# Kernel tuning notes

Hardware: AMD Instinct MI355X
Metric: run time of the kernel (lower is better)

The kernel has to match this reference:

```python
import jax, jax.numpy as jnp
import numpy as np

N_NODES = 50000
N_EDGES = 400000
N_GRAPHS = 128
IN_DIM = 768
HID = 128
N_CLASSES = 11
BN_EPS = 1e-5


def _sage_conv(x, src, dst, Wl, bl, Wr):
    # PyG SAGEConv (aggr='mean'): out = lin_l(mean_{j->i} x_j) + lin_r(x_i)
    # messages flow src -> dst; nodes with no in-edges get a zero aggregate.
    n = x.shape[0]
    deg = jax.ops.segment_sum(jnp.ones_like(dst, x.dtype), dst, num_segments=n)
    agg = jax.ops.segment_sum(x[src], dst, num_segments=n)  # [N, d] gather+scatter
    agg = agg / jnp.maximum(deg, 1.0)[:, None]
    return agg @ Wl.T + bl + x @ Wr.T


def _batch_norm(x, gamma, beta):
    # training-mode BatchNorm1d: biased batch statistics over the node axis
    m = jnp.mean(x, axis=0)
    v = jnp.var(x, axis=0)
    return (x - m) * jax.lax.rsqrt(v + BN_EPS) * gamma + beta


def setup_inputs() -> dict:
    key = jax.random.key(0)
    ks = jax.random.split(key, 16)
    x = jax.random.normal(ks[0], (N_NODES, IN_DIM), dtype=jnp.float32)
    edge_index = jax.random.randint(ks[1], (2, N_EDGES), 0, N_NODES, dtype=jnp.int32)
    batch = jnp.sort(jax.random.randint(ks[2], (N_NODES,), 0, N_GRAPHS, dtype=jnp.int32))

    def lin_w(k, out_d, in_d):
        return jax.random.normal(k, (out_d, in_d), dtype=jnp.float32) * (1.0 / np.sqrt(in_d))

    params = {
        'W1l': lin_w(ks[3], HID, IN_DIM), 'b1': jnp.zeros((HID,), jnp.float32),
        'W1r': lin_w(ks[4], HID, IN_DIM),
        'g1': jnp.ones((HID,), jnp.float32), 'be1': jnp.zeros((HID,), jnp.float32),
        'W2l': lin_w(ks[5], HID, HID), 'b2': jnp.zeros((HID,), jnp.float32),
        'W2r': lin_w(ks[6], HID, HID),
        'g2': jnp.ones((HID,), jnp.float32), 'be2': jnp.zeros((HID,), jnp.float32),
        'W3l': lin_w(ks[7], HID, HID), 'b3': jnp.zeros((HID,), jnp.float32),
        'W3r': lin_w(ks[8], HID, HID),
        'g3': jnp.ones((HID,), jnp.float32), 'be3': jnp.zeros((HID,), jnp.float32),
        'Wlin': lin_w(ks[9], N_CLASSES, HID), 'blin': jnp.zeros((N_CLASSES,), jnp.float32),
    }
    return {'x': x, 'edge_index': edge_index, 'batch': batch, **params}


def reference(x, edge_index, batch,
              W1l, b1, W1r, g1, be1,
              W2l, b2, W2r, g2, be2,
              W3l, b3, W3r, g3, be3,
              Wlin, blin):
    src, dst = edge_index[0], edge_index[1]
    h = jax.nn.relu(_batch_norm(_sage_conv(x, src, dst, W1l, b1, W1r), g1, be1))
    h = jax.nn.relu(_batch_norm(_sage_conv(h, src, dst, W2l, b2, W2r), g2, be2))
    h = _batch_norm(_sage_conv(h, src, dst, W3l, b3, W3r), g3, be3)
    # global_max_pool over graph ids
    pooled = jax.ops.segment_max(h, batch, num_segments=N_GRAPHS)  # [G, HID]
    # dropout is identity at inference
    return pooled @ Wlin.T + blin  # [G, 11]
```

## Files before the change

### kernel.cpp

```cpp
#include <hip/hip_runtime.h>

#define N_NODESC 50000
#define N_EDGESC 400000
#define N_GRAPHSC 128
#define IN_DIMC 768
#define HIDC 128
#define NCLSC 11
#define BN_EPSC 1e-5f
#define NB_AGG 8
#define NREP 64
#define SCAN_NB ((N_NODESC + 255) / 256)

typedef __bf16 bf16_t;
typedef __bf16 bf16x2 __attribute__((ext_vector_type(2)));
typedef __bf16 bf16x8 __attribute__((ext_vector_type(8)));
typedef float f32x4 __attribute__((ext_vector_type(4)));

typedef __attribute__((address_space(1))) void glb_void;
typedef __attribute__((address_space(3))) void lds_void;

__device__ __forceinline__ void cp16(const void* g, void* l) {
    __builtin_amdgcn_global_load_lds((glb_void*)g, (lds_void*)l, 16, 0, 0);
}

__device__ __forceinline__ f32x4 mfma_16x16x32_bf16(bf16x8 a, bf16x8 b, f32x4 c) {
    return __builtin_amdgcn_mfma_f32_16x16x32_bf16(a, b, c, 0, 0, 0);
}

template<int MODE, int KC>
__global__ __launch_bounds__(256) void gemm_kernel(const void* __restrict__ Av,
                                                   const bf16_t* __restrict__ Wb,
                                                   const float* __restrict__ sc,
                                                   bf16_t* __restrict__ Cl,
                                                   bf16_t* __restrict__ Cr,
                                                   int M)
{
    constexpr int NK   = KC / 32;
    constexpr int ASZ  = (MODE == 0) ? 16384 : 8192;
    constexpr int BSZ  = 8192;
    constexpr int NBB  = (MODE == 0) ? 2 : 3;
    constexpr int AISS = (MODE == 0) ? 4 : 2;
    constexpr int AKB  = (MODE == 0) ? 128 : 64;
    constexpr int SCSZ = (MODE == 1) ? 1024 : 0;
    __shared__ __align__(16) unsigned char smem[3 * ASZ + NBB * BSZ + SCSZ];
    unsigned char* Asm = smem;
    unsigned char* Bsm = smem + 3 * ASZ;
    float* scS = (float*)(smem + 3 * ASZ + NBB * BSZ);

    const int t    = threadIdx.x;
    const int m0   = blockIdx.x * 128;
    const int half = blockIdx.y;
    const int wid  = t >> 6;
    const int lane = t & 63;
    const int wm   = (wid >> 1) * 64;
    const int wn   = (wid & 1) * 64;
    const int l16  = lane & 15;
    const int quad = lane >> 4;

    const char* aSrc[AISS]; int aDst[AISS];
#pragma unroll
    for (int s = 0; s < AISS; s++) {
        int L = (s * 4 + wid) * 64 + lane;
        int r, c;
        if (MODE == 0) { r = L >> 3; c = (L & 7) ^ (r & 7); }
        else           { r = L >> 2; c = (L & 3) ^ ((r >> 1) & 3); }
        int row = m0 + r; if (row > M - 1) row = M - 1;
        if (MODE == 0) aSrc[s] = (const char*)Av + ((size_t)row * KC + (size_t)c * 4) * 4;
        else           aSrc[s] = (const char*)Av + ((size_t)row * KC + (size_t)c * 8) * 2;
        aDst[s] = (s * 4 + wid) * 1024;
    }
    const char* bSrc[2]; int bDst[2];
#pragma unroll
    for (int s = 0; s < 2; s++) {
        int L = (s * 4 + wid) * 64 + lane;
        int r = L >> 2;
        int c = (L & 3) ^ ((r >> 1) & 3);
        bSrc[s] = (const char*)(Wb + (size_t)(half * 128 + r) * KC + c * 8);
        bDst[s] = (s * 4 + wid) * 1024;
    }

    int aOff[4][2], bOff[4];
#pragma unroll
    for (int i = 0; i < 4; i++) {
        int ra = wm + i * 16 + l16;
        if (MODE == 0) {
            aOff[i][0] = ra * 128 + (((2 * quad)     ^ (ra & 7)) * 16);
            aOff[i][1] = ra * 128 + (((2 * quad + 1) ^ (ra & 7)) * 16);
        } else {
            aOff[i][0] = ra * 64 + ((quad ^ ((ra >> 1) & 3)) * 16);
            aOff[i][1] = 0;
        }
        int rb = wn + i * 16 + l16;
        bOff[i] = rb * 64 + ((quad ^ ((rb >> 1) & 3)) * 16);
    }

    if (MODE == 1) {
        scS[t] = sc[t];
        __syncthreads();
    }

#pragma unroll
    for (int s = 0; s < AISS; s++) cp16(aSrc[s], Asm + aDst[s]);
#pragma unroll
    for (int s = 0; s < 2; s++)    cp16(bSrc[s], Bsm + bDst[s]);
#pragma unroll
    for (int s = 0; s < AISS; s++) cp16(aSrc[s] + AKB, Asm + ASZ + aDst[s]);
    if (MODE == 1) {
#pragma unroll
        for (int s = 0; s < 2; s++) cp16(bSrc[s] + 64, Bsm + BSZ + bDst[s]);
    }

    f32x4 acc[4][4] = {};

    for (int it = 0; it < NK; ++it) {
        if (it + 2 < NK) {
            if constexpr (MODE == 0) {
                const size_t kb1 = (size_t)(it + 1) * 64;
                const int bb = (it + 1) & 1;
#pragma unroll
                for (int s = 0; s < 2; s++) cp16(bSrc[s] + kb1, Bsm + bb * BSZ + bDst[s]);
                const size_t ka2 = (size_t)(it + 2) * 128;
                const int ab = (it + 2) % 3;
#pragma unroll
                for (int s = 0; s < 4; s++) cp16(aSrc[s] + ka2, Asm + ab * ASZ + aDst[s]);
                asm volatile("s_waitcnt vmcnt(10)" ::: "memory");
            } else {
                const size_t kb2 = (size_t)(it + 2) * 64;
                const int nb = (it + 2) % 3;
#pragma unroll
                for (int s = 0; s < 2; s++) cp16(aSrc[s] + kb2, Asm + nb * ASZ + aDst[s]);
#pragma unroll
                for (int s = 0; s < 2; s++) cp16(bSrc[s] + kb2, Bsm + nb * BSZ + bDst[s]);
                asm volatile("s_waitcnt vmcnt(8)" ::: "memory");
            }
        } else if (it + 1 < NK) {
            if constexpr (MODE == 0) {
                const size_t kb1 = (size_t)(it + 1) * 64;
                const int bb = (it + 1) & 1;
#pragma unroll
                for (int s = 0; s < 2; s++) cp16(bSrc[s] + kb1, Bsm + bb * BSZ + bDst[s]);
                asm volatile("s_waitcnt vmcnt(6)" ::: "memory");
            } else {
                asm volatile("s_waitcnt vmcnt(4)" ::: "memory");
            }
        } else {
            asm volatile("s_waitcnt vmcnt(0)" ::: "memory");
        }
        asm volatile("s_barrier" ::: "memory");

        const unsigned char* Ab = Asm + (it % 3) * ASZ;
        const unsigned char* Bb = Bsm + ((MODE == 0) ? (it & 1) : (it % 3)) * BSZ;
        bf16x8 af[4], bfr[4];
        if constexpr (MODE == 0) {
#pragma unroll
            for (int i = 0; i < 4; i++) {
                float4 u0 = *(const float4*)(Ab + aOff[i][0]);
                float4 u1 = *(const float4*)(Ab + aOff[i][1]);
                af[i][0] = (bf16_t)u0.x; af[i][1] = (bf16_t)u0.y;
                af[i][2] = (bf16_t)u0.z; af[i][3] = (bf16_t)u0.w;
                af[i][4] = (bf16_t)u1.x; af[i][5] = (bf16_t)u1.y;
                af[i][6] = (bf16_t)u1.z; af[i][7] = (bf16_t)u1.w;
            }
        } else {
            float4 s0 = *(const float4*)&scS[it * 32 + quad * 8];
            float4 s1 = *(const float4*)&scS[it * 32 + quad * 8 + 4];
            float4 h0 = *(const float4*)&scS[HIDC + it * 32 + quad * 8];
            float4 h1 = *(const float4*)&scS[HIDC + it * 32 + quad * 8 + 4];
            float ss[8] = {s0.x, s0.y, s0.z, s0.w, s1.x, s1.y, s1.z, s1.w};
            float hh[8] = {h0.x, h0.y, h0.z, h0.w, h1.x, h1.y, h1.z, h1.w};
#pragma unroll
            for (int i = 0; i < 4; i++) {
                bf16x8 raw = *(const bf16x8*)(Ab + aOff[i][0]);
#pragma unroll
                for (int e = 0; e < 8; e++)
                    af[i][e] = (bf16_t)fmaxf(fmaf((float)raw[e], ss[e], hh[e]), 0.0f);
            }
        }
#pragma unroll
        for (int j = 0; j < 4; j++)
            bfr[j] = *(const bf16x8*)(Bb + bOff[j]);
#pragma unroll
        for (int i = 0; i < 4; i++)
#pragma unroll
            for (int j = 0; j < 4; j++)
                acc[i][j] = mfma_16x16x32_bf16(af[i], bfr[j], acc[i][j]);

        asm volatile("s_barrier" ::: "memory");
    }

    bf16_t* C = half ? Cr : Cl;
#pragma unroll
    for (int i = 0; i < 4; i++) {
        int rowb = m0 + wm + i * 16 + quad * 4;
#pragma unroll
        for (int j = 0; j < 4; j++) {
            int colh = wn + j * 16 + l16;
#pragma unroll
            for (int rr = 0; rr < 4; rr++) {
                int row = rowb + rr;
                if (row < M) C[(size_t)row * HIDC + colh] = (bf16_t)acc[i][j][rr];
            }
        }
    }
}

__global__ void init_kernel(const float* __restrict__ W1l, const float* __restrict__ W1r,
                            const float* __restrict__ W2l, const float* __restrict__ W2r,
                            const float* __restrict__ W3l, const float* __restrict__ W3r,
                            bf16_t* __restrict__ Wb1, bf16_t* __restrict__ Wb2,
                            bf16_t* __restrict__ Wb3,
                            int* __restrict__ degi, float* __restrict__ stats)
{
    const int NW1 = 128 * IN_DIMC;
    const int NW2 = 128 * HIDC;
    const int NS  = 3 * NREP * 256;
    int j = blockIdx.x * blockDim.x + threadIdx.x;
    if (j < 2 * NW1) { Wb1[j] = (bf16_t)((j < NW1) ? W1l[j] : W1r[j - NW1]); return; }
    j -= 2 * NW1;
    if (j < 2 * NW2) { Wb2[j] = (bf16_t)((j < NW2) ? W2l[j] : W2r[j - NW2]); return; }
    j -= 2 * NW2;
    if (j < 2 * NW2) { Wb3[j] = (bf16_t)((j < NW2) ? W3l[j] : W3r[j - NW2]); return; }
    j -= 2 * NW2;
    if (j < NS) { stats[j] = 0.0f; return; }
    j -= NS;
    if (j < N_NODESC) degi[j] = 0;
}

__global__ void degi_kernel(const int* __restrict__ ei, int* __restrict__ degi) {
    int e = blockIdx.x * blockDim.x + threadIdx.x;
    if (e < N_EDGESC) atomicAdd(&degi[ei[N_EDGESC + e]], 1);
}

__global__ __launch_bounds__(256) void scan1_kernel(const int* __restrict__ degi,
                                                    int* __restrict__ local,
                                                    int* __restrict__ partials)
{
    __shared__ int tmp[256];
    const int t = threadIdx.x;
    const int i = blockIdx.x * 256 + t;
    int v = (i < N_NODESC) ? degi[i] : 0;
    tmp[t] = v;
    __syncthreads();
    for (int off = 1; off < 256; off <<= 1) {
        int u = (t >= off) ? tmp[t - off] : 0;
        __syncthreads();
        tmp[t] += u;
        __syncthreads();
    }
    if (i < N_NODESC) local[i] = tmp[t] - v;
    if (t == 255) partials[blockIdx.x] = tmp[255];
}

__global__ __launch_bounds__(256) void scan2_kernel(int* __restrict__ partials)
{
    __shared__ int tmp[256];
    const int t = threadIdx.x;
    int v = (t < SCAN_NB) ? partials[t] : 0;
    tmp[t] = v;
    __syncthreads();
    for (int off = 1; off < 256; off <<= 1) {
        int u = (t >= off) ? tmp[t - off] : 0;
        __syncthreads();
        tmp[t] += u;
        __syncthreads();
    }
    if (t < SCAN_NB) partials[t] = tmp[t] - v;
}

__global__ __launch_bounds__(256) void scan3_kernel(const int* __restrict__ local,
                                                    const int* __restrict__ partials,
                                                    int* __restrict__ rowptr,
                                                    int* __restrict__ cursor)
{
    const int i = blockIdx.x * 256 + threadIdx.x;
    if (i < N_NODESC) {
        int r = local[i] + partials[blockIdx.x];
        rowptr[i] = r;
        cursor[i] = r;
    }
    if (i == 0) rowptr[N_NODESC] = N_EDGESC;
}

__global__ void fill_kernel(const int* __restrict__ ei, int* __restrict__ cursor,
                            int* __restrict__ col) {
    int e = blockIdx.x * blockDim.x + threadIdx.x;
    if (e >= N_EDGESC) return;
    int d = ei[N_EDGESC + e];
    int pos = atomicAdd(&cursor[d], 1);
    col[pos] = ei[e];
}

__global__ __launch_bounds__(128) void agg_combine_kernel(const int* __restrict__ rowptr,
                                                          const int* __restrict__ col,
                                                          const bf16_t* __restrict__ Plb,
                                                          const bf16_t* __restrict__ Prb,
                                                          const float* __restrict__ bias,
                                                          bf16_t* __restrict__ Hb,
                                                          float* __restrict__ stats, int M)
{
    const int lane = threadIdx.x & 63;
    const int wv   = threadIdx.x >> 6;
    const int c0   = lane * 2;
    const float b0 = bias[c0], b1v = bias[c0 + 1];
    float s0 = 0.f, s1 = 0.f, q0 = 0.f, q1 = 0.f;
    const int n0 = blockIdx.x * NB_AGG + wv * (NB_AGG / 2);
    for (int rr = 0; rr < NB_AGG / 2; rr++) {
        int n = n0 + rr;
        if (n >= M) break;
        int lo = rowptr[n], hi = rowptr[n + 1];
        float a0 = 0.f, a1 = 0.f;
        for (int e = lo; e < hi; e += 8) {
            int rem = hi - e;
            int idx[8];
#pragma unroll
            for (int j = 0; j < 8; j++) {
                int ee = e + j; if (ee > hi - 1) ee = hi - 1;
                idx[j] = col[ee];
            }
            bf16x2 v[8];
#pragma unroll
            for (int j = 0; j < 8; j++)
                v[j] = *(const bf16x2*)&Plb[(size_t)idx[j] * HIDC + c0];
#pragma unroll
            for (int j = 0; j < 8; j++)
                if (j < rem) { a0 += (float)v[j][0]; a1 += (float)v[j][1]; }
        }
        int d = hi - lo;
        float inv = 1.0f / (float)(d > 0 ? d : 1);
        bf16x2 pr = *(const bf16x2*)&Prb[(size_t)n * HIDC + c0];
        float pre0 = fmaf(a0, inv, b0) + (float)pr[0];
        float pre1 = fmaf(a1, inv, b1v) + (float)pr[1];
        bf16x2 hv; hv[0] = (bf16_t)pre0; hv[1] = (bf16_t)pre1;
        *(bf16x2*)&Hb[(size_t)n * HIDC + c0] = hv;
        s0 += pre0; s1 += pre1; q0 += pre0 * pre0; q1 += pre1 * pre1;
    }
    const int rep = (blockIdx.x * 2 + wv) & (NREP - 1);
    atomicAdd(&stats[rep * 256 + c0], s0);
    atomicAdd(&stats[rep * 256 + c0 + 1], s1);
    atomicAdd(&stats[rep * 256 + HIDC + c0], q0);
    atomicAdd(&stats[rep * 256 + HIDC + c0 + 1], q1);
}

__global__ __launch_bounds__(128) void finalize_kernel(const float* __restrict__ stats,
                                                       const float* __restrict__ g,
                                                       const float* __restrict__ be,
                                                       float* __restrict__ sc, int M)
{
    int c = threadIdx.x;
    float sum = 0.f, sumsq = 0.f;
    for (int r = 0; r < NREP; r++) {
        sum   += stats[r * 256 + c];
        sumsq += stats[r * 256 + HIDC + c];
    }
    float invM = 1.0f / (float)M;
    float mean = sum * invM;
    float var  = sumsq * invM - mean * mean;
    float s = rsqrtf(var + BN_EPSC) * g[c];
    sc[c] = s;
    sc[HIDC + c] = be[c] - mean * s;
}

__global__ __launch_bounds__(128) void poolhead_kernel(const bf16_t* __restrict__ Hb,
                                                       const float* __restrict__ sc,
                                                       const int* __restrict__ batch,
                                                       const float* __restrict__ Wlin,
                                                       const float* __restrict__ blin,
                                                       float* __restrict__ out, int M)
{
    __shared__ float sp[HIDC];
    int gph = blockIdx.x;
    int c   = threadIdx.x;
    float s = sc[c], h = sc[HIDC + c];
    int lo = 0, hi = M;
    while (lo < hi) { int m = (lo + hi) >> 1; if (batch[m] < gph) lo = m + 1; else hi = m; }
    int lo2 = lo, hi2 = M;
    while (lo2 < hi2) { int m = (lo2 + hi2) >> 1; if (batch[m] < gph + 1) lo2 = m + 1; else hi2 = m; }
    float mx = -INFINITY;
    for (int rr = lo; rr < lo2; rr++)
        mx = fmaxf(mx, fmaf((float)Hb[(size_t)rr * HIDC + c], s, h));
    sp[c] = mx;
    __syncthreads();
    if (c < NCLSC) {
        float acc = blin[c];
        for (int k = 0; k < HIDC; k++) acc += sp[k] * Wlin[c * HIDC + k];
        out[gph * NCLSC + c] = acc;
    }
}

extern "C" void kernel_launch(void* const* d_in, const int* in_sizes, int n_in,
                              void* d_out, int out_size, void* d_ws, size_t ws_size,
                              hipStream_t stream)
{
    const float* x     = (const float*)d_in[0];
    const int*   ei    = (const int*)d_in[1];
    const int*   batch = (const int*)d_in[2];
    const float* W1l = (const float*)d_in[3];
    const float* b1  = (const float*)d_in[4];
    const float* W1r = (const float*)d_in[5];
    const float* g1  = (const float*)d_in[6];
    const float* be1 = (const float*)d_in[7];
    const float* W2l = (const float*)d_in[8];
    const float* b2  = (const float*)d_in[9];
    const float* W2r = (const float*)d_in[10];
    const float* g2  = (const float*)d_in[11];
    const float* be2 = (const float*)d_in[12];
    const float* W3l = (const float*)d_in[13];
    const float* b3  = (const float*)d_in[14];
    const float* W3r = (const float*)d_in[15];
    const float* g3  = (const float*)d_in[16];
    const float* be3 = (const float*)d_in[17];
    const float* Wlin = (const float*)d_in[18];
    const float* blin = (const float*)d_in[19];

    const int M = N_NODESC;

    char* w = (char*)d_ws;
    bf16_t* Plb  = (bf16_t*)w;  w += (size_t)M * HIDC * 2;
    bf16_t* Prb  = (bf16_t*)w;  w += (size_t)M * HIDC * 2;
    bf16_t* Hb   = (bf16_t*)w;  w += (size_t)M * HIDC * 2;
    bf16_t* Wb1  = (bf16_t*)w;  w += (size_t)256 * IN_DIMC * 2;
    bf16_t* Wb2  = (bf16_t*)w;  w += (size_t)256 * HIDC * 2;
    bf16_t* Wb3  = (bf16_t*)w;  w += (size_t)256 * HIDC * 2;
    int*   rowptr= (int*)w;     w += (size_t)(M + 16) * 4;
    int*   col   = (int*)w;     w += (size_t)N_EDGESC * 4;
    int*   cursor= (int*)w;     w += (size_t)M * 4;
    int*   degi  = (int*)w;     w += (size_t)M * 4;
    int*   slocal= (int*)w;     w += (size_t)M * 4;
    int*   spart = (int*)w;     w += 256 * 4;
    float* stats = (float*)w;   w += (size_t)3 * NREP * 256 * 4;
    float* sc    = (float*)w;   w += 3 * 256 * 4;

    float* stats1 = stats;
    float* stats2 = stats + NREP * 256;
    float* stats3 = stats + 2 * NREP * 256;
    float* sc1 = sc, *sc2 = sc + 256, *sc3 = sc + 512;

    const dim3 gemm_grid((M + 127) / 128, 2);
    const int agg_blocks = (M + NB_AGG - 1) / NB_AGG;
    const int init_total = 2 * 128 * IN_DIMC + 4 * 128 * HIDC + 3 * NREP * 256 + M;

    init_kernel<<<(init_total + 255) / 256, 256, 0, stream>>>(W1l, W1r, W2l, W2r, W3l, W3r,
                                                              Wb1, Wb2, Wb3, degi, stats);
    degi_kernel<<<(N_EDGESC + 255) / 256, 256, 0, stream>>>(ei, degi);
    scan1_kernel<<<SCAN_NB, 256, 0, stream>>>(degi, slocal, spart);
    scan2_kernel<<<1, 256, 0, stream>>>(spart);
    scan3_kernel<<<SCAN_NB, 256, 0, stream>>>(slocal, spart, rowptr, cursor);
    fill_kernel<<<(N_EDGESC + 255) / 256, 256, 0, stream>>>(ei, cursor, col);

    gemm_kernel<0, IN_DIMC><<<gemm_grid, 256, 0, stream>>>(x, Wb1, nullptr, Plb, Prb, M);
    agg_combine_kernel<<<agg_blocks, 128, 0, stream>>>(rowptr, col, Plb, Prb, b1, Hb, stats1, M);
    finalize_kernel<<<1, 128, 0, stream>>>(stats1, g1, be1, sc1, M);

    gemm_kernel<1, HIDC><<<gemm_grid, 256, 0, stream>>>(Hb, Wb2, sc1, Plb, Prb, M);
    agg_combine_kernel<<<agg_blocks, 128, 0, stream>>>(rowptr, col, Plb, Prb, b2, Hb, stats2, M);
    finalize_kernel<<<1, 128, 0, stream>>>(stats2, g2, be2, sc2, M);

    gemm_kernel<1, HIDC><<<gemm_grid, 256, 0, stream>>>(Hb, Wb3, sc2, Plb, Prb, M);
    agg_combine_kernel<<<agg_blocks, 128, 0, stream>>>(rowptr, col, Plb, Prb, b3, Hb, stats3, M);
    finalize_kernel<<<1, 128, 0, stream>>>(stats3, g3, be3, sc3, M);

    poolhead_kernel<<<N_GRAPHSC, 128, 0, stream>>>(Hb, sc3, batch, Wlin, blin, (float*)d_out, M);
}
```

Measured before the change: 587.0 us.

## Fuse BN finalize and scan2 into consumers, restructure layer-1 GEMM pipeline

```diff
diff --git a/kernel.cpp b/kernel.cpp
--- a/kernel.cpp
+++ b/kernel.cpp
@@ -30,7 +30,9 @@
 template<int MODE, int KC>
 __global__ __launch_bounds__(256) void gemm_kernel(const void* __restrict__ Av,
                                                    const bf16_t* __restrict__ Wb,
-                                                   const float* __restrict__ sc,
+                                                   const float* __restrict__ stats,
+                                                   const float* __restrict__ g,
+                                                   const float* __restrict__ be,
                                                    bf16_t* __restrict__ Cl,
                                                    bf16_t* __restrict__ Cr,
                                                    int M)
@@ -38,14 +40,15 @@
     constexpr int NK   = KC / 32;
     constexpr int ASZ  = (MODE == 0) ? 16384 : 8192;
     constexpr int BSZ  = 8192;
+    constexpr int NAB  = (MODE == 0) ? 2 : 3;
     constexpr int NBB  = (MODE == 0) ? 2 : 3;
     constexpr int AISS = (MODE == 0) ? 4 : 2;
     constexpr int AKB  = (MODE == 0) ? 128 : 64;
-    constexpr int SCSZ = (MODE == 1) ? 1024 : 0;
-    __shared__ __align__(16) unsigned char smem[3 * ASZ + NBB * BSZ + SCSZ];
+    constexpr int SCSZ = (MODE == 1) ? 1024 : 16;
+    __shared__ __align__(16) unsigned char smem[NAB * ASZ + NBB * BSZ + SCSZ];
     unsigned char* Asm = smem;
-    unsigned char* Bsm = smem + 3 * ASZ;
-    float* scS = (float*)(smem + 3 * ASZ + NBB * BSZ);
+    unsigned char* Bsm = smem + NAB * ASZ;
+    float* scS = (float*)(smem + NAB * ASZ + NBB * BSZ);
 
     const int t    = threadIdx.x;
     const int m0   = blockIdx.x * 128;
@@ -95,63 +98,48 @@
     }
 
     if (MODE == 1) {
-        scS[t] = sc[t];
+        if (t < HIDC) {
+            float sum = 0.f, sumsq = 0.f;
+            for (int r = 0; r < NREP; r++) {
+                sum   += stats[r * 256 + t];
+                sumsq += stats[r * 256 + HIDC + t];
+            }
+            float invM = 1.0f / (float)M;
+            float mean = sum * invM;
+            float var  = sumsq * invM - mean * mean;
+            float s = rsqrtf(var + BN_EPSC) * g[t];
+            scS[t] = s;
+            scS[HIDC + t] = be[t] - mean * s;
+        }
         __syncthreads();
     }
 
-#pragma unroll
-    for (int s = 0; s < AISS; s++) cp16(aSrc[s], Asm + aDst[s]);
-#pragma unroll
-    for (int s = 0; s < 2; s++)    cp16(bSrc[s], Bsm + bDst[s]);
-#pragma unroll
-    for (int s = 0; s < AISS; s++) cp16(aSrc[s] + AKB, Asm + ASZ + aDst[s]);
-    if (MODE == 1) {
-#pragma unroll
-        for (int s = 0; s < 2; s++) cp16(bSrc[s] + 64, Bsm + BSZ + bDst[s]);
-    }
-
     f32x4 acc[4][4] = {};
 
-    for (int it = 0; it < NK; ++it) {
-        if (it + 2 < NK) {
-            if constexpr (MODE == 0) {
-                const size_t kb1 = (size_t)(it + 1) * 64;
-                const int bb = (it + 1) & 1;
-#pragma unroll
-                for (int s = 0; s < 2; s++) cp16(bSrc[s] + kb1, Bsm + bb * BSZ + bDst[s]);
-                const size_t ka2 = (size_t)(it + 2) * 128;
-                const int ab = (it + 2) % 3;
-#pragma unroll
-                for (int s = 0; s < 4; s++) cp16(aSrc[s] + ka2, Asm + ab * ASZ + aDst[s]);
-                asm volatile("s_waitcnt vmcnt(10)" ::: "memory");
-            } else {
-                const size_t kb2 = (size_t)(it + 2) * 64;
-                const int nb = (it + 2) % 3;
-#pragma unroll
-                for (int s = 0; s < 2; s++) cp16(aSrc[s] + kb2, Asm + nb * ASZ + aDst[s]);
-#pragma unroll
-                for (int s = 0; s < 2; s++) cp16(bSrc[s] + kb2, Bsm + nb * BSZ + bDst[s]);
-                asm volatile("s_waitcnt vmcnt(8)" ::: "memory");
-            }
-        } else if (it + 1 < NK) {
-            if constexpr (MODE == 0) {
-                const size_t kb1 = (size_t)(it + 1) * 64;
-                const int bb = (it + 1) & 1;
-#pragma unroll
-                for (int s = 0; s < 2; s++) cp16(bSrc[s] + kb1, Bsm + bb * BSZ + bDst[s]);
+    if constexpr (MODE == 0) {
+#pragma unroll
+        for (int s = 0; s < 4; s++) cp16(aSrc[s], Asm + aDst[s]);
+#pragma unroll
+        for (int s = 0; s < 2; s++) cp16(bSrc[s], Bsm + bDst[s]);
+
+        for (int it = 0; it < NK; ++it) {
+            if (it + 1 < NK) {
+                const size_t ka = (size_t)(it + 1) * 128;
+                const size_t kb = (size_t)(it + 1) * 64;
+                const int nb = (it + 1) & 1;
+#pragma unroll
+                for (int s = 0; s < 4; s++) cp16(aSrc[s] + ka, Asm + nb * ASZ + aDst[s]);
+#pragma unroll
+                for (int s = 0; s < 2; s++) cp16(bSrc[s] + kb, Bsm + nb * BSZ + bDst[s]);
                 asm volatile("s_waitcnt vmcnt(6)" ::: "memory");
             } else {
-                asm volatile("s_waitcnt vmcnt(4)" ::: "memory");
-            }
-        } else {
-            asm volatile("s_waitcnt vmcnt(0)" ::: "memory");
-        }
-        asm volatile("s_barrier" ::: "memory");
-
-        const unsigned char* Ab = Asm + (it % 3) * ASZ;
-        const unsigned char* Bb = Bsm + ((MODE == 0) ? (it & 1) : (it % 3)) * BSZ;
-        bf16x8 af[4], bfr[4];
-        if constexpr (MODE == 0) {
+                asm volatile("s_waitcnt vmcnt(0)" ::: "memory");
+            }
+            asm volatile("s_barrier" ::: "memory");
+
+            const unsigned char* Ab = Asm + (it & 1) * ASZ;
+            const unsigned char* Bb = Bsm + (it & 1) * BSZ;
+            bf16x8 af[4], bfr[4];
 #pragma unroll
             for (int i = 0; i < 4; i++) {
                 float4 u0 = *(const float4*)(Ab + aOff[i][0]);
@@ -161,7 +149,46 @@
                 af[i][4] = (bf16_t)u1.x; af[i][5] = (bf16_t)u1.y;
                 af[i][6] = (bf16_t)u1.z; af[i][7] = (bf16_t)u1.w;
             }
-        } else {
+#pragma unroll
+            for (int j = 0; j < 4; j++)
+                bfr[j] = *(const bf16x8*)(Bb + bOff[j]);
+#pragma unroll
+            for (int i = 0; i < 4; i++)
+#pragma unroll
+                for (int j = 0; j < 4; j++)
+                    acc[i][j] = mfma_16x16x32_bf16(af[i], bfr[j], acc[i][j]);
+
+            asm volatile("s_barrier" ::: "memory");
+        }
+    } else {
+#pragma unroll
+        for (int s = 0; s < 2; s++) cp16(aSrc[s], Asm + aDst[s]);
+#pragma unroll
+        for (int s = 0; s < 2; s++) cp16(bSrc[s], Bsm + bDst[s]);
+#pragma unroll
+        for (int s = 0; s < 2; s++) cp16(aSrc[s] + 64, Asm + ASZ + aDst[s]);
+#pragma unroll
+        for (int s = 0; s < 2; s++) cp16(bSrc[s] + 64, Bsm + BSZ + bDst[s]);
+
+        for (int it = 0; it < NK; ++it) {
+            if (it + 2 < NK) {
+                const size_t kb2 = (size_t)(it + 2) * 64;
+                const int nb = (it + 2) % 3;
+#pragma unroll
+                for (int s = 0; s < 2; s++) cp16(aSrc[s] + kb2, Asm + nb * ASZ + aDst[s]);
+#pragma unroll
+                for (int s = 0; s < 2; s++) cp16(bSrc[s] + kb2, Bsm + nb * BSZ + bDst[s]);
+                asm volatile("s_waitcnt vmcnt(8)" ::: "memory");
+            } else if (it + 1 < NK) {
+                asm volatile("s_waitcnt vmcnt(4)" ::: "memory");
+            } else {
+                asm volatile("s_waitcnt vmcnt(0)" ::: "memory");
+            }
+            asm volatile("s_barrier" ::: "memory");
+
+            const unsigned char* Ab = Asm + (it % 3) * ASZ;
+            const unsigned char* Bb = Bsm + (it % 3) * BSZ;
+            bf16x8 af[4], bfr[4];
             float4 s0 = *(const float4*)&scS[it * 32 + quad * 8];
             float4 s1 = *(const float4*)&scS[it * 32 + quad * 8 + 4];
             float4 h0 = *(const float4*)&scS[HIDC + it * 32 + quad * 8];
@@ -175,17 +202,17 @@
                 for (int e = 0; e < 8; e++)
                     af[i][e] = (bf16_t)fmaxf(fmaf((float)raw[e], ss[e], hh[e]), 0.0f);
             }
-        }
-#pragma unroll
-        for (int j = 0; j < 4; j++)
-            bfr[j] = *(const bf16x8*)(Bb + bOff[j]);
-#pragma unroll
-        for (int i = 0; i < 4; i++)
 #pragma unroll
             for (int j = 0; j < 4; j++)
-                acc[i][j] = mfma_16x16x32_bf16(af[i], bfr[j], acc[i][j]);
-
-        asm volatile("s_barrier" ::: "memory");
+                bfr[j] = *(const bf16x8*)(Bb + bOff[j]);
+#pragma unroll
+            for (int i = 0; i < 4; i++)
+#pragma unroll
+                for (int j = 0; j < 4; j++)
+                    acc[i][j] = mfma_16x16x32_bf16(af[i], bfr[j], acc[i][j]);
+
+            asm volatile("s_barrier" ::: "memory");
+        }
     }
 
     bf16_t* C = half ? Cr : Cl;
@@ -251,30 +278,27 @@
     if (t == 255) partials[blockIdx.x] = tmp[255];
 }
 
-__global__ __launch_bounds__(256) void scan2_kernel(int* __restrict__ partials)
-{
-    __shared__ int tmp[256];
-    const int t = threadIdx.x;
-    int v = (t < SCAN_NB) ? partials[t] : 0;
-    tmp[t] = v;
-    __syncthreads();
-    for (int off = 1; off < 256; off <<= 1) {
-        int u = (t >= off) ? tmp[t - off] : 0;
-        __syncthreads();
-        tmp[t] += u;
-        __syncthreads();
-    }
-    if (t < SCAN_NB) partials[t] = tmp[t] - v;
-}
-
 __global__ __launch_bounds__(256) void scan3_kernel(const int* __restrict__ local,
                                                     const int* __restrict__ partials,
                                                     int* __restrict__ rowptr,
                                                     int* __restrict__ cursor)
 {
-    const int i = blockIdx.x * 256 + threadIdx.x;
+    __shared__ int inc[256];
+    __shared__ int orig[256];
+    const int t = threadIdx.x;
+    int v = (t < SCAN_NB) ? partials[t] : 0;
+    inc[t] = v; orig[t] = v;
+    __syncthreads();
+    for (int off = 1; off < 256; off <<= 1) {
+        int u = (t >= off) ? inc[t - off] : 0;
+        __syncthreads();
+        inc[t] += u;
+        __syncthreads();
+    }
+    const int boff = inc[blockIdx.x] - orig[blockIdx.x];
+    const int i = blockIdx.x * 256 + t;
     if (i < N_NODESC) {
-        int r = local[i] + partials[blockIdx.x];
+        int r = local[i] + boff;
         rowptr[i] = r;
         cursor[i] = r;
     }
@@ -341,12 +365,18 @@
     atomicAdd(&stats[rep * 256 + HIDC + c0 + 1], q1);
 }
 
-__global__ __launch_bounds__(128) void finalize_kernel(const float* __restrict__ stats,
+__global__ __launch_bounds__(128) void poolhead_kernel(const bf16_t* __restrict__ Hb,
+                                                       const float* __restrict__ stats,
                                                        const float* __restrict__ g,
                                                        const float* __restrict__ be,
-                                                       float* __restrict__ sc, int M)
-{
-    int c = threadIdx.x;
+                                                       const int* __restrict__ batch,
+                                                       const float* __restrict__ Wlin,
+                                                       const float* __restrict__ blin,
+                                                       float* __restrict__ out, int M)
+{
+    __shared__ float sp[HIDC];
+    int gph = blockIdx.x;
+    int c   = threadIdx.x;
     float sum = 0.f, sumsq = 0.f;
     for (int r = 0; r < NREP; r++) {
         sum   += stats[r * 256 + c];
@@ -356,21 +386,8 @@
     float mean = sum * invM;
     float var  = sumsq * invM - mean * mean;
     float s = rsqrtf(var + BN_EPSC) * g[c];
-    sc[c] = s;
-    sc[HIDC + c] = be[c] - mean * s;
-}
-
-__global__ __launch_bounds__(128) void poolhead_kernel(const bf16_t* __restrict__ Hb,
-                                                       const float* __restrict__ sc,
-                                                       const int* __restrict__ batch,
-                                                       const float* __restrict__ Wlin,
-                                                       const float* __restrict__ blin,
-                                                       float* __restrict__ out, int M)
-{
-    __shared__ float sp[HIDC];
-    int gph = blockIdx.x;
-    int c   = threadIdx.x;
-    float s = sc[c], h = sc[HIDC + c];
+    float h = be[c] - mean * s;
+
     int lo = 0, hi = M;
     while (lo < hi) { int m = (lo + hi) >> 1; if (batch[m] < gph) lo = m + 1; else hi = m; }
     int lo2 = lo, hi2 = M;
@@ -428,12 +445,10 @@
     int*   slocal= (int*)w;     w += (size_t)M * 4;
     int*   spart = (int*)w;     w += 256 * 4;
     float* stats = (float*)w;   w += (size_t)3 * NREP * 256 * 4;
-    float* sc    = (float*)w;   w += 3 * 256 * 4;
 
     float* stats1 = stats;
     float* stats2 = stats + NREP * 256;
     float* stats3 = stats + 2 * NREP * 256;
-    float* sc1 = sc, *sc2 = sc + 256, *sc3 = sc + 512;
 
     const dim3 gemm_grid((M + 127) / 128, 2);
     const int agg_blocks = (M + NB_AGG - 1) / NB_AGG;
@@ -443,21 +458,19 @@
                                                               Wb1, Wb2, Wb3, degi, stats);
     degi_kernel<<<(N_EDGESC + 255) / 256, 256, 0, stream>>>(ei, degi);
     scan1_kernel<<<SCAN_NB, 256, 0, stream>>>(degi, slocal, spart);
-    scan2_kernel<<<1, 256, 0, stream>>>(spart);
     scan3_kernel<<<SCAN_NB, 256, 0, stream>>>(slocal, spart, rowptr, cursor);
     fill_kernel<<<(N_EDGESC + 255) / 256, 256, 0, stream>>>(ei, cursor, col);
 
-    gemm_kernel<0, IN_DIMC><<<gemm_grid, 256, 0, stream>>>(x, Wb1, nullptr, Plb, Prb, M);
+    gemm_kernel<0, IN_DIMC><<<gemm_grid, 256, 0, stream>>>(x, Wb1, nullptr, nullptr, nullptr,
+                                                           Plb, Prb, M);
     agg_combine_kernel<<<agg_blocks, 128, 0, stream>>>(rowptr, col, Plb, Prb, b1, Hb, stats1, M);
-    finalize_kernel<<<1, 128, 0, stream>>>(stats1, g1, be1, sc1, M);
-
-    gemm_kernel<1, HIDC><<<gemm_grid, 256, 0, stream>>>(Hb, Wb2, sc1, Plb, Prb, M);
+
+    gemm_kernel<1, HIDC><<<gemm_grid, 256, 0, stream>>>(Hb, Wb2, stats1, g1, be1, Plb, Prb, M);
     agg_combine_kernel<<<agg_blocks, 128, 0, stream>>>(rowptr, col, Plb, Prb, b2, Hb, stats2, M);
-    finalize_kernel<<<1, 128, 0, stream>>>(stats2, g2, be2, sc2, M);
-
-    gemm_kernel<1, HIDC><<<gemm_grid, 256, 0, stream>>>(Hb, Wb3, sc2, Plb, Prb, M);
+
+    gemm_kernel<1, HIDC><<<gemm_grid, 256, 0, stream>>>(Hb, Wb3, stats2, g2, be2, Plb, Prb, M);
     agg_combine_kernel<<<agg_blocks, 128, 0, stream>>>(rowptr, col, Plb, Prb, b3, Hb, stats3, M);
-    finalize_kernel<<<1, 128, 0, stream>>>(stats3, g3, be3, sc3, M);
-
-    poolhead_kernel<<<N_GRAPHSC, 128, 0, stream>>>(Hb, sc3, batch, Wlin, blin, (float*)d_out, M);
-}
+
+    poolhead_kernel<<<N_GRAPHSC, 128, 0, stream>>>(Hb, stats3, g3, be3, batch, Wlin, blin,
+                                                   (float*)d_out, M);
+}
```

Result: faster. 574.5 us (-2.1%).
